# Optimization experiments

Measured on AMD Instinct MI355X. Metric: run time of the kernel, lower is better.

The kernel has to match this reference:

```python
import jax, jax.numpy as jnp
import numpy as np

B, NB, H, C = 32, 1024, 768, 64


def setup_inputs() -> dict:
    key = jax.random.key(0)
    k1, k2, k3, k4, k5, k6 = jax.random.split(key, 6)
    block_tokens = jax.random.normal(k1, (B, NB, H), dtype=jnp.float32)
    block_active = jax.random.randint(k2, (B, NB), 0, 2) == 1
    block_to_channel_map = jax.random.randint(k3, (NB,), 0, C, dtype=jnp.int64)
    # agg_gate params: Linear(H, H//2) -> Tanh -> Linear(H//2, 1)
    s1 = 1.0 / np.sqrt(H)
    s2 = 1.0 / np.sqrt(H // 2)
    W1 = jax.random.uniform(k4, (H, H // 2), jnp.float32, -s1, s1)
    b1 = jnp.zeros((H // 2,), jnp.float32)
    W2 = jax.random.uniform(k5, (H // 2, 1), jnp.float32, -s2, s2)
    b2 = jnp.zeros((1,), jnp.float32)
    return {"block_tokens": block_tokens, "block_active": block_active,
            "block_to_channel_map": block_to_channel_map,
            "W1": W1, "b1": b1, "W2": W2, "b2": b2}


def reference(block_tokens, block_active, block_to_channel_map, W1, b1, W2, b2):
    # gate MLP: (B, NB)
    h = jnp.tanh(jnp.einsum('bnh,hk->bnk', block_tokens, W1) + b1)
    gate = (jnp.einsum('bnk,ko->bno', h, W2) + b2).squeeze(-1)  # (B, NB)

    # (C, NB) one-hot channel membership; (B, C, NB) active-per-channel mask
    onehot = block_to_channel_map[None, :] == jnp.arange(C)[:, None]
    mask = block_active[:, None, :] & onehot[None, :, :]  # (B, C, NB)

    neg_inf = jnp.float32(-jnp.inf)
    g = jnp.where(mask, gate[:, None, :], neg_inf)  # (B, C, NB)
    m = jnp.max(g, axis=-1, keepdims=True)
    m_safe = jnp.where(jnp.isfinite(m), m, 0.0)  # guard all-masked channels
    e = jnp.where(mask, jnp.exp(g - m_safe), 0.0)
    s = jnp.sum(e, axis=-1, keepdims=True)
    w = jnp.where(s > 0, e / jnp.where(s > 0, s, 1.0), 0.0)  # softmax, nan->0

    channel_tokens = jnp.einsum('bcn,bnh->bch', w, block_tokens)  # (B, C, H)
    channel_active = jnp.any(mask, axis=-1)  # (B, C)
    return channel_tokens, channel_active
```

## Files before the change

### kernel.cpp

```cpp
#include <hip/hip_runtime.h>
#include <math.h>

#define B_   32
#define NB_  1024
#define H_   768
#define K_   384
#define C_   64

#define ROWS_   128
#define NSTEP_  (H_ / 32)
#define NT_     (K_ / 16)

typedef __attribute__((ext_vector_type(8))) short  bf16x8;
typedef __attribute__((ext_vector_type(4))) float  f32x4;

__device__ __forceinline__ short f2bf(float f) {
    unsigned u = __float_as_uint(f);
    unsigned r = (u + 0x7fffu + ((u >> 16) & 1u)) >> 16;
    return (short)r;
}

__global__ __launch_bounds__(256) void prep_w1(const float* __restrict__ W1,
                                               short* __restrict__ swz)
{
    int idx = blockIdx.x * 256 + threadIdx.x;
    int k = idx / K_, n = idx % K_;
    float v = W1[idx];
    int s = k >> 5, g = (k >> 3) & 3, i = k & 7;
    int t = n >> 4, nn = n & 15;
    swz[((s * 24 + t) * 512) + (g * 16 + nn) * 8 + i] = f2bf(v);
}

__global__ __launch_bounds__(512, 2) void gate_kernel(
    const float* __restrict__ tokens, const short* __restrict__ swz,
    const float* __restrict__ b1, const float* __restrict__ W2,
    const float* __restrict__ b2, float* __restrict__ gate)
{
    __shared__ short As[2][8 * 512];
    __shared__ short Bs[2][24 * 512];
    __shared__ float red[8][128];

    const int tid  = threadIdx.x;
    const int lane = tid & 63;
    const int w    = tid >> 6;
    const int row0 = blockIdx.x * ROWS_;

    const int arow = tid >> 2;
    const int akc  = tid & 3;
    const size_t agbase = (size_t)(row0 + arow) * H_ + akc * 8;
    const int    aoff   = (arow >> 4) * 512 + (akc * 16 + (arow & 15)) * 8;

    f32x4 acc[8][3];
#pragma unroll
    for (int f = 0; f < 8; ++f)
#pragma unroll
        for (int j = 0; j < 3; ++j) acc[f][j] = (f32x4){0.f, 0.f, 0.f, 0.f};

    {
        float4 pa0 = *(const float4*)(tokens + agbase);
        float4 pa1 = *(const float4*)(tokens + agbase + 4);
        float4 pb0 = *(const float4*)((const char*)swz + 0 * 8192 + tid * 16);
        float4 pb1 = *(const float4*)((const char*)swz + 1 * 8192 + tid * 16);
        float4 pb2 = *(const float4*)((const char*)swz + 2 * 8192 + tid * 16);
        bf16x8 av = { f2bf(pa0.x), f2bf(pa0.y), f2bf(pa0.z), f2bf(pa0.w),
                      f2bf(pa1.x), f2bf(pa1.y), f2bf(pa1.z), f2bf(pa1.w) };
        *(bf16x8*)&As[0][aoff] = av;
        *(float4*)&Bs[0][0 * 4096 + tid * 8] = pb0;
        *(float4*)&Bs[0][1 * 4096 + tid * 8] = pb1;
        *(float4*)&Bs[0][2 * 4096 + tid * 8] = pb2;
    }
    __syncthreads();

    int buf = 0;
    for (int s = 0; s < NSTEP_; ++s) {
        float4 pa0, pa1, pb0, pb1, pb2;
        if (s < NSTEP_ - 1) {
            const size_t ga = agbase + (size_t)(s + 1) * 32;
            pa0 = *(const float4*)(tokens + ga);
            pa1 = *(const float4*)(tokens + ga + 4);
            const char* gb = (const char*)swz + (size_t)(s + 1) * 24576;
            pb0 = *(const float4*)(gb + 0 * 8192 + tid * 16);
            pb1 = *(const float4*)(gb + 1 * 8192 + tid * 16);
            pb2 = *(const float4*)(gb + 2 * 8192 + tid * 16);
        }

        bf16x8 af[8];
#pragma unroll
        for (int f = 0; f < 8; ++f)
            af[f] = *(bf16x8*)&As[buf][f * 512 + lane * 8];
#pragma unroll
        for (int j = 0; j < 3; ++j) {
            bf16x8 bv = *(bf16x8*)&Bs[buf][(w * 3 + j) * 512 + lane * 8];
#pragma unroll
            for (int f = 0; f < 8; ++f)
                acc[f][j] = __builtin_amdgcn_mfma_f32_16x16x32_bf16(
                                af[f], bv, acc[f][j], 0, 0, 0);
        }

        if (s < NSTEP_ - 1) {
            bf16x8 av = { f2bf(pa0.x), f2bf(pa0.y), f2bf(pa0.z), f2bf(pa0.w),
                          f2bf(pa1.x), f2bf(pa1.y), f2bf(pa1.z), f2bf(pa1.w) };
            *(bf16x8*)&As[buf ^ 1][aoff] = av;
            *(float4*)&Bs[buf ^ 1][0 * 4096 + tid * 8] = pb0;
            *(float4*)&Bs[buf ^ 1][1 * 4096 + tid * 8] = pb1;
            *(float4*)&Bs[buf ^ 1][2 * 4096 + tid * 8] = pb2;
        }
        __syncthreads();
        buf ^= 1;
    }

    float ps[8][4];
#pragma unroll
    for (int f = 0; f < 8; ++f)
#pragma unroll
        for (int r = 0; r < 4; ++r) ps[f][r] = 0.f;

#pragma unroll
    for (int j = 0; j < 3; ++j) {
        const int n  = (w * 3 + j) * 16 + (lane & 15);
        const float bb = b1[n];
        const float ww = W2[n];
#pragma unroll
        for (int f = 0; f < 8; ++f)
#pragma unroll
            for (int r = 0; r < 4; ++r)
                ps[f][r] += tanhf(acc[f][j][r] + bb) * ww;
    }
#pragma unroll
    for (int m = 1; m < 16; m <<= 1)
#pragma unroll
        for (int f = 0; f < 8; ++f)
#pragma unroll
            for (int r = 0; r < 4; ++r)
                ps[f][r] += __shfl_xor(ps[f][r], m, 64);

    if ((lane & 15) == 0) {
        const int rbase = (lane >> 4) * 4;
#pragma unroll
        for (int f = 0; f < 8; ++f)
#pragma unroll
            for (int r = 0; r < 4; ++r)
                red[w][f * 16 + rbase + r] = ps[f][r];
    }
    __syncthreads();
    if (tid < ROWS_) {
        float sgate = b2[0];
#pragma unroll
        for (int ww2 = 0; ww2 < 8; ++ww2) sgate += red[ww2][tid];
        gate[row0 + tid] = sgate;
    }
}

__global__ __launch_bounds__(256) void agg_kernel(
    const float* __restrict__ tokens, const int* __restrict__ active,
    const int* __restrict__ cmap, const float* __restrict__ gate,
    float* __restrict__ out_tok, float* __restrict__ out_act)
{
    __shared__ float wls[NB_];
    __shared__ float red[256];
    __shared__ int   idxs[NB_];
    __shared__ float wts[NB_];
    __shared__ int   gbase[17];

    const int b = blockIdx.x >> 6, c = blockIdx.x & 63;
    const int tid = threadIdx.x, lane = tid & 63, wid = tid >> 6;

    float lmax = -INFINITY;
    for (int n = tid; n < NB_; n += 256) {
        const bool msk = (active[b * NB_ + n] != 0) && (cmap[n] == c);
        const float g  = msk ? gate[b * NB_ + n] : -INFINITY;
        wls[n] = g;
        lmax = fmaxf(lmax, g);
    }
    red[tid] = lmax; __syncthreads();
    for (int s = 128; s > 0; s >>= 1) {
        if (tid < s) red[tid] = fmaxf(red[tid], red[tid + s]);
        __syncthreads();
    }
    const float m = red[0]; __syncthreads();
    const float msafe = (m > -INFINITY) ? m : 0.f;

    float lsum = 0.f;
    for (int n = tid; n < NB_; n += 256) {
        const float g = wls[n];
        const float e = (g > -INFINITY) ? __expf(g - msafe) : 0.f;
        wls[n] = e; lsum += e;
    }
    red[tid] = lsum; __syncthreads();
    for (int s = 128; s > 0; s >>= 1) {
        if (tid < s) red[tid] += red[tid + s];
        __syncthreads();
    }
    const float ssum = red[0];
    const float inv  = (ssum > 0.f) ? 1.f / ssum : 0.f;
    __syncthreads();

#pragma unroll
    for (int it = 0; it < 4; ++it) {
        const int n = it * 256 + wid * 64 + lane;
        const unsigned long long mask = __ballot(wls[n] > 0.f);
        if (lane == 0) gbase[1 + it * 4 + wid] = __popcll(mask);
    }
    __syncthreads();
    if (tid == 0) {
        gbase[0] = 0;
        for (int i = 1; i <= 16; ++i) gbase[i] += gbase[i - 1];
    }
    __syncthreads();
#pragma unroll
    for (int it = 0; it < 4; ++it) {
        const int n = it * 256 + wid * 64 + lane;
        const float e = wls[n];
        const unsigned long long mask = __ballot(e > 0.f);
        if (e > 0.f) {
            const int pos = gbase[it * 4 + wid] +
                            __popcll(mask & ((1ull << lane) - 1ull));
            idxs[pos] = n;
            wts[pos]  = e * inv;
        }
    }
    __syncthreads();
    const int cnt = gbase[16];

    float a0 = 0.f, a1 = 0.f, a2 = 0.f;
    const float* tb = tokens + (size_t)b * NB_ * H_;
    for (int i = 0; i < cnt; ++i) {
        const float wv = wts[i];
        const float* t = tb + (size_t)idxs[i] * H_;
        a0 += wv * t[tid];
        a1 += wv * t[tid + 256];
        a2 += wv * t[tid + 512];
    }
    float* o = out_tok + ((size_t)(b * C_ + c)) * H_;
    o[tid]       = a0;
    o[tid + 256] = a1;
    o[tid + 512] = a2;
    if (tid == 0) out_act[b * C_ + c] = (m > -INFINITY) ? 1.f : 0.f;
}

extern "C" void kernel_launch(void* const* d_in, const int* in_sizes, int n_in,
                              void* d_out, int out_size, void* d_ws, size_t ws_size,
                              hipStream_t stream)
{
    const float* tokens = (const float*)d_in[0];
    const int*   active = (const int*)  d_in[1];
    const int*   cmap   = (const int*)  d_in[2];
    const float* W1     = (const float*)d_in[3];
    const float* b1     = (const float*)d_in[4];
    const float* W2     = (const float*)d_in[5];
    const float* b2     = (const float*)d_in[6];

    float* out      = (float*)d_out;
    float* out_act  = out + (size_t)B_ * C_ * H_;

    short* swz     = (short*)d_ws;
    float* gate_ws = (float*)((char*)d_ws + 589824);

    prep_w1<<<(H_ * K_) / 256, 256, 0, stream>>>(W1, swz);
    gate_kernel<<<(B_ * NB_) / ROWS_, 512, 0, stream>>>(tokens, swz, b1, W2, b2, gate_ws);
    agg_kernel<<<B_ * C_, 256, 0, stream>>>(tokens, active, cmap, gate_ws, out, out_act);
}
```

Before: 66.69 us.

## Compute gate only for active blocks, restructure gate GEMM pipeline and tanh

Adds a compaction kernel that builds a per-batch list of active block indices. The gate GEMM now runs only over active rows and skips chunks past the active count. The GEMM also changes shape: B fragments come straight from global memory into registers instead of LDS, the A tile in LDS is XOR-swizzled, loads are prefetched two steps ahead, and raw barriers replace __syncthreads. tanhf is replaced with an exp/rcp approximation. Together these aim to cut roughly half the MLP FLOPs and token reads, at the cost of an extra launch, gathered row loads and lower tanh accuracy.

```diff
diff --git a/kernel.cpp b/kernel.cpp
--- a/kernel.cpp
+++ b/kernel.cpp
@@ -1,23 +1,25 @@
 #include <hip/hip_runtime.h>
 #include <math.h>
 
-#define B_   32
-#define NB_  1024
-#define H_   768
-#define K_   384
-#define C_   64
-
-#define ROWS_   128
-#define NSTEP_  (H_ / 32)
-#define NT_     (K_ / 16)
-
-typedef __attribute__((ext_vector_type(8))) short  bf16x8;
-typedef __attribute__((ext_vector_type(4))) float  f32x4;
+#define B_    32
+#define NB_   1024
+#define H_    768
+#define K_    384
+#define C_    64
+#define ROWS_ 128
+#define NSTEP_ 24
+
+typedef __attribute__((ext_vector_type(8))) short bf16x8;
+typedef __attribute__((ext_vector_type(4))) float f32x4;
 
 __device__ __forceinline__ short f2bf(float f) {
     unsigned u = __float_as_uint(f);
     unsigned r = (u + 0x7fffu + ((u >> 16) & 1u)) >> 16;
     return (short)r;
+}
+__device__ __forceinline__ float ftanh(float x) {
+    float e = __expf(2.f * x);
+    return 1.f - 2.f * __builtin_amdgcn_rcpf(e + 1.f);
 }
 
 __global__ __launch_bounds__(256) void prep_w1(const float* __restrict__ W1,
@@ -31,100 +33,129 @@
     swz[((s * 24 + t) * 512) + (g * 16 + nn) * 8 + i] = f2bf(v);
 }
 
-__global__ __launch_bounds__(512, 2) void gate_kernel(
+__global__ __launch_bounds__(1024) void compact_kernel(
+    const int* __restrict__ active, int* __restrict__ list, int* __restrict__ cnt)
+{
+    __shared__ int wsum[16];
+    __shared__ int wbase[17];
+    const int b = blockIdx.x, tid = threadIdx.x, lane = tid & 63, wid = tid >> 6;
+    const int flag = active[b * NB_ + tid] != 0;
+    const unsigned long long m = __ballot(flag);
+    if (lane == 0) wsum[wid] = __popcll(m);
+    __syncthreads();
+    if (tid == 0) {
+        int r = 0;
+        for (int i = 0; i < 16; ++i) { wbase[i] = r; r += wsum[i]; }
+        wbase[16] = r;
+        cnt[b] = r;
+    }
+    __syncthreads();
+    const int total = wbase[16];
+    if (flag) {
+        const int pos = wbase[wid] + __popcll(m & ((1ull << lane) - 1ull));
+        list[b * NB_ + pos] = tid;
+    }
+    if (tid >= total) list[b * NB_ + tid] = 0;
+}
+
+__global__ __launch_bounds__(512) void gate_kernel(
     const float* __restrict__ tokens, const short* __restrict__ swz,
     const float* __restrict__ b1, const float* __restrict__ W2,
-    const float* __restrict__ b2, float* __restrict__ gate)
-{
-    __shared__ short As[2][8 * 512];
-    __shared__ short Bs[2][24 * 512];
+    const float* __restrict__ b2, const int* __restrict__ list,
+    const int* __restrict__ cnt, float* __restrict__ gate)
+{
+    __shared__ __align__(16) short As[2][4096];
     __shared__ float red[8][128];
 
-    const int tid  = threadIdx.x;
+    const int b = blockIdx.x >> 3;
+    const int chunk = blockIdx.x & 7;
+    if (chunk * ROWS_ >= cnt[b]) return;
+
+    const int tid = threadIdx.x;
     const int lane = tid & 63;
-    const int w    = tid >> 6;
-    const int row0 = blockIdx.x * ROWS_;
+    const int w = tid >> 6;
 
     const int arow = tid >> 2;
     const int akc  = tid & 3;
-    const size_t agbase = (size_t)(row0 + arow) * H_ + akc * 8;
-    const int    aoff   = (arow >> 4) * 512 + (akc * 16 + (arow & 15)) * 8;
-
-    f32x4 acc[8][3];
+    const int nrow = list[b * NB_ + chunk * ROWS_ + arow];
+    const float* aptr = tokens + ((size_t)b * NB_ + nrow) * H_ + akc * 8;
+
+    const int aoff = (arow >> 4) * 512 + (((akc * 16 + (arow & 15)) ^ (akc * 2)) * 8);
+    const int roff = (lane ^ ((lane >> 4) * 2)) * 8;
+    const short* bbase = swz + (w * 3) * 512 + lane * 8;
+
+    f32x4 acc[3][8];
+#pragma unroll
+    for (int j = 0; j < 3; ++j)
+#pragma unroll
+        for (int f = 0; f < 8; ++f) acc[j][f] = (f32x4){0.f, 0.f, 0.f, 0.f};
+
+    float4 pe0 = *(const float4*)(aptr);
+    float4 pe1 = *(const float4*)(aptr + 4);
+    float4 po0 = *(const float4*)(aptr + 32);
+    float4 po1 = *(const float4*)(aptr + 36);
+    bf16x8 be0 = *(const bf16x8*)(bbase);
+    bf16x8 be1 = *(const bf16x8*)(bbase + 512);
+    bf16x8 be2 = *(const bf16x8*)(bbase + 1024);
+    bf16x8 bo0 = be0, bo1 = be1, bo2 = be2;
+    {
+        bf16x8 av = {f2bf(pe0.x), f2bf(pe0.y), f2bf(pe0.z), f2bf(pe0.w),
+                     f2bf(pe1.x), f2bf(pe1.y), f2bf(pe1.z), f2bf(pe1.w)};
+        *(bf16x8*)&As[0][aoff] = av;
+    }
+    asm volatile("s_waitcnt lgkmcnt(0)" ::: "memory");
+    __builtin_amdgcn_s_barrier();
+    __builtin_amdgcn_sched_barrier(0);
+
+#define GATE_ITER(S, PA0, PA1, QA0, QA1, BC0, BC1, BC2, BN0, BN1, BN2)        \
+    do {                                                                      \
+        if ((S) + 2 < NSTEP_) {                                               \
+            PA0 = *(const float4*)(aptr + ((S) + 2) * 32);                    \
+            PA1 = *(const float4*)(aptr + ((S) + 2) * 32 + 4);                \
+        }                                                                     \
+        if ((S) + 1 < NSTEP_) {                                               \
+            const short* bp = bbase + ((S) + 1) * 12288;                      \
+            BN0 = *(const bf16x8*)(bp);                                       \
+            BN1 = *(const bf16x8*)(bp + 512);                                 \
+            BN2 = *(const bf16x8*)(bp + 1024);                                \
+            bf16x8 av = {f2bf(QA0.x), f2bf(QA0.y), f2bf(QA0.z), f2bf(QA0.w),  \
+                         f2bf(QA1.x), f2bf(QA1.y), f2bf(QA1.z), f2bf(QA1.w)}; \
+            *(bf16x8*)&As[((S) + 1) & 1][aoff] = av;                          \
+        }                                                                     \
+        _Pragma("unroll")                                                     \
+        for (int f = 0; f < 8; ++f) {                                         \
+            bf16x8 af = *(const bf16x8*)&As[(S) & 1][f * 512 + roff];         \
+            acc[0][f] = __builtin_amdgcn_mfma_f32_16x16x32_bf16(af, BC0, acc[0][f], 0, 0, 0); \
+            acc[1][f] = __builtin_amdgcn_mfma_f32_16x16x32_bf16(af, BC1, acc[1][f], 0, 0, 0); \
+            acc[2][f] = __builtin_amdgcn_mfma_f32_16x16x32_bf16(af, BC2, acc[2][f], 0, 0, 0); \
+        }                                                                     \
+        asm volatile("s_waitcnt lgkmcnt(0)" ::: "memory");                    \
+        __builtin_amdgcn_s_barrier();                                         \
+        __builtin_amdgcn_sched_barrier(0);                                    \
+    } while (0)
+
+    for (int s = 0; s < NSTEP_; s += 2) {
+        GATE_ITER(s,     pe0, pe1, po0, po1, be0, be1, be2, bo0, bo1, bo2);
+        GATE_ITER(s + 1, po0, po1, pe0, pe1, bo0, bo1, bo2, be0, be1, be2);
+    }
+#undef GATE_ITER
+
+    float ps[8][4];
 #pragma unroll
     for (int f = 0; f < 8; ++f)
 #pragma unroll
-        for (int j = 0; j < 3; ++j) acc[f][j] = (f32x4){0.f, 0.f, 0.f, 0.f};
-
-    {
-        float4 pa0 = *(const float4*)(tokens + agbase);
-        float4 pa1 = *(const float4*)(tokens + agbase + 4);
-        float4 pb0 = *(const float4*)((const char*)swz + 0 * 8192 + tid * 16);
-        float4 pb1 = *(const float4*)((const char*)swz + 1 * 8192 + tid * 16);
-        float4 pb2 = *(const float4*)((const char*)swz + 2 * 8192 + tid * 16);
-        bf16x8 av = { f2bf(pa0.x), f2bf(pa0.y), f2bf(pa0.z), f2bf(pa0.w),
-                      f2bf(pa1.x), f2bf(pa1.y), f2bf(pa1.z), f2bf(pa1.w) };
-        *(bf16x8*)&As[0][aoff] = av;
-        *(float4*)&Bs[0][0 * 4096 + tid * 8] = pb0;
-        *(float4*)&Bs[0][1 * 4096 + tid * 8] = pb1;
-        *(float4*)&Bs[0][2 * 4096 + tid * 8] = pb2;
-    }
-    __syncthreads();
-
-    int buf = 0;
-    for (int s = 0; s < NSTEP_; ++s) {
-        float4 pa0, pa1, pb0, pb1, pb2;
-        if (s < NSTEP_ - 1) {
-            const size_t ga = agbase + (size_t)(s + 1) * 32;
-            pa0 = *(const float4*)(tokens + ga);
-            pa1 = *(const float4*)(tokens + ga + 4);
-            const char* gb = (const char*)swz + (size_t)(s + 1) * 24576;
-            pb0 = *(const float4*)(gb + 0 * 8192 + tid * 16);
-            pb1 = *(const float4*)(gb + 1 * 8192 + tid * 16);
-            pb2 = *(const float4*)(gb + 2 * 8192 + tid * 16);
-        }
-
-        bf16x8 af[8];
-#pragma unroll
-        for (int f = 0; f < 8; ++f)
-            af[f] = *(bf16x8*)&As[buf][f * 512 + lane * 8];
-#pragma unroll
-        for (int j = 0; j < 3; ++j) {
-            bf16x8 bv = *(bf16x8*)&Bs[buf][(w * 3 + j) * 512 + lane * 8];
-#pragma unroll
-            for (int f = 0; f < 8; ++f)
-                acc[f][j] = __builtin_amdgcn_mfma_f32_16x16x32_bf16(
-                                af[f], bv, acc[f][j], 0, 0, 0);
-        }
-
-        if (s < NSTEP_ - 1) {
-            bf16x8 av = { f2bf(pa0.x), f2bf(pa0.y), f2bf(pa0.z), f2bf(pa0.w),
-                          f2bf(pa1.x), f2bf(pa1.y), f2bf(pa1.z), f2bf(pa1.w) };
-            *(bf16x8*)&As[buf ^ 1][aoff] = av;
-            *(float4*)&Bs[buf ^ 1][0 * 4096 + tid * 8] = pb0;
-            *(float4*)&Bs[buf ^ 1][1 * 4096 + tid * 8] = pb1;
-            *(float4*)&Bs[buf ^ 1][2 * 4096 + tid * 8] = pb2;
-        }
-        __syncthreads();
-        buf ^= 1;
-    }
-
-    float ps[8][4];
-#pragma unroll
-    for (int f = 0; f < 8; ++f)
-#pragma unroll
         for (int r = 0; r < 4; ++r) ps[f][r] = 0.f;
 
 #pragma unroll
     for (int j = 0; j < 3; ++j) {
-        const int n  = (w * 3 + j) * 16 + (lane & 15);
+        const int n = (w * 3 + j) * 16 + (lane & 15);
         const float bb = b1[n];
         const float ww = W2[n];
 #pragma unroll
         for (int f = 0; f < 8; ++f)
 #pragma unroll
             for (int r = 0; r < 4; ++r)
-                ps[f][r] += tanhf(acc[f][j][r] + bb) * ww;
+                ps[f][r] += ftanh(acc[j][f][r] + bb) * ww;
     }
 #pragma unroll
     for (int m = 1; m < 16; m <<= 1)
@@ -144,10 +175,10 @@
     }
     __syncthreads();
     if (tid < ROWS_) {
-        float sgate = b2[0];
-#pragma unroll
-        for (int ww2 = 0; ww2 < 8; ++ww2) sgate += red[ww2][tid];
-        gate[row0 + tid] = sgate;
+        float sg = b2[0];
+#pragma unroll
+        for (int q = 0; q < 8; ++q) sg += red[q][tid];
+        gate[b * NB_ + list[b * NB_ + chunk * ROWS_ + tid]] = sg;
     }
 }
 
@@ -255,8 +286,11 @@
 
     short* swz     = (short*)d_ws;
     float* gate_ws = (float*)((char*)d_ws + 589824);
-
+    int*   list    = (int*)  ((char*)d_ws + 720896);
+    int*   cntb    = (int*)  ((char*)d_ws + 851968);
+
+    compact_kernel<<<B_, 1024, 0, stream>>>(active, list, cntb);
     prep_w1<<<(H_ * K_) / 256, 256, 0, stream>>>(W1, swz);
-    gate_kernel<<<(B_ * NB_) / ROWS_, 512, 0, stream>>>(tokens, swz, b1, W2, b2, gate_ws);
+    gate_kernel<<<B_ * 8, 512, 0, stream>>>(tokens, swz, b1, W2, b2, list, cntb, gate_ws);
     agg_kernel<<<B_ * C_, 256, 0, stream>>>(tokens, active, cmap, gate_ws, out, out_act);
 }
```

Result: faster. 55.94 us (-16.1%).
